# Optimization experiments

Hardware: AMD Instinct MI355X
Metric: run time of the kernel (lower is better)

## Reference

```python
import jax, jax.numpy as jnp
import numpy as np

B, IN_C, H, W = 32, 256, 32, 32
C_OUT, NUM_MODES, NEG_MODES, EMB = 256, 1, 3, 512
SIGMA, BETA, NEG_SCOPE, EPS = 0.5, 0.3, 2.0, 1e-12


def _l2norm(v, axis):
    return v / jnp.maximum(jnp.linalg.norm(v, axis=axis, keepdims=True), EPS)


def setup_inputs() -> dict:
    key = jax.random.key(0)
    ks = jax.random.split(key, 6)
    x = jax.random.normal(ks[0], (B, IN_C, H, W), jnp.float32)
    W_emb = jax.random.normal(ks[1], (EMB, IN_C), jnp.float32) * 0.02  # 1x1 conv kernel
    # rep_fc / neg_rep_fc: nn.Linear(1, C*modes*E), normal_init std=0.01
    rep_w = jax.random.normal(ks[2], (C_OUT * NUM_MODES * EMB, 1), jnp.float32) * 0.01
    rep_b = jax.random.normal(ks[3], (C_OUT * NUM_MODES * EMB,), jnp.float32) * 0.01
    neg_rep_w = jax.random.normal(ks[4], (C_OUT * NEG_MODES * EMB, 1), jnp.float32) * 0.01
    neg_rep_b = jax.random.normal(ks[5], (C_OUT * NEG_MODES * EMB,), jnp.float32) * 0.01
    return {"x": x, "W_emb": W_emb, "rep_w": rep_w, "rep_b": rep_b,
            "neg_rep_w": neg_rep_w, "neg_rep_b": neg_rep_b}


def reference(x, W_emb, rep_w, rep_b, neg_rep_w, neg_rep_b):
    # emb_module: 1x1 conv, then L2-normalize over channel dim (dim=1)
    emb = jnp.einsum('bchw,ec->behw', x, W_emb)
    emb = _l2norm(emb, axis=1)                                    # [B,E,H,W], unit-norm over E
    # training branch: reps = normalize(rep_fc(1.0)) = normalize(w*1 + b)
    reps = _l2norm((rep_w[:, 0] + rep_b).reshape(C_OUT, NUM_MODES, EMB), axis=2)
    reps_neg = _l2norm((neg_rep_w[:, 0] + neg_rep_b).reshape(C_OUT, NEG_MODES, EMB), axis=2)

    def dist(r):
        # ||e - r||^2 = ||e||^2 + ||r||^2 - 2 e.r = 2 - 2 e.r (both unit-norm)
        dot = jnp.einsum('behw,cme->bcmhw', emb, r)               # [B,C,M,H,W]
        return jnp.sqrt(jnp.maximum(2.0 - 2.0 * dot, 0.0))

    distances = dist(reps)                                        # [B,C,1,H,W]
    distances_neg = dist(reps_neg)                                # [B,C,3,H,W]
    inv2s2 = 1.0 / (2.0 * SIGMA ** 2)

    probs_neg = jnp.exp(-distances_neg ** 2 * inv2s2)
    cls_score_neg = probs_neg.max(axis=2)                         # [B,C,H,W]
    probs_ori = jnp.exp(-distances ** 2 * inv2s2).max(axis=2)     # [B,C,H,W]

    neg_min = distances_neg.min(axis=2, keepdims=True)            # [B,C,1,H,W]
    probs = jnp.exp(-(distances + BETA * jax.nn.relu(NEG_SCOPE - neg_min)) ** 2 * inv2s2)
    # cls_norm=True branch
    probs_sumj = probs.sum(axis=2)                                # [B,C,H,W]
    cls_score = probs_sumj / probs_sumj.sum(axis=1, keepdims=True)
    return (cls_score, cls_score_neg, distances, distances_neg, probs_ori)
```

## Files before the change

kernel.cpp:

```cpp
#include <hip/hip_runtime.h>
#include <stdint.h>

using s16x8 = __attribute__((ext_vector_type(8))) short;
using f32x4 = __attribute__((ext_vector_type(4))) float;

#define HW 1024
#define INC 256
#define EMB 512

#define OFF_CS 0
#define OFF_CN 8388608
#define OFF_D  16777216
#define OFF_DN 25165824
#define OFF_PO 50331648

__device__ __forceinline__ uint32_t f2bf(float f) {
  uint32_t u = __float_as_uint(f);
  return (u + 0x7FFFu + ((u >> 16) & 1u)) >> 16;
}
__device__ __forceinline__ int lswz(int row, int byte) {
  return byte ^ (((row >> 2) & 7) << 4);
}
__device__ __forceinline__ void gload16(const void* g, void* l) {
  __builtin_amdgcn_global_load_lds((const __attribute__((address_space(1))) uint32_t*)g,
                                   (__attribute__((address_space(3))) uint32_t*)l, 16, 0, 0);
}

__global__ __launch_bounds__(64) void k_prep(
    const float* __restrict__ rep_w, const float* __restrict__ rep_b,
    const float* __restrict__ neg_w, const float* __restrict__ neg_b,
    uint16_t* __restrict__ R, float* __restrict__ norms, float* __restrict__ psum) {
  int rb = blockIdx.x, lane = threadIdx.x;
  if (lane < 32) { norms[rb * 32 + lane] = 0.f; psum[rb * 32 + lane] = 0.f; }
  int c = rb >> 2, md = rb & 3;
  const float* w  = (md == 0) ? rep_w : neg_w;
  const float* bb = (md == 0) ? rep_b : neg_b;
  int base = (md == 0) ? c * EMB : (c * 3 + md - 1) * EMB;
  float v[8]; float ss = 0.f;
#pragma unroll
  for (int j = 0; j < 8; ++j) {
    float t = w[base + lane * 8 + j] + bb[base + lane * 8 + j];
    v[j] = t; ss += t * t;
  }
#pragma unroll
  for (int o = 1; o < 64; o <<= 1) ss += __shfl_xor(ss, o, 64);
  float inv = 1.f / fmaxf(sqrtf(ss), 1e-12f);
  uint16_t* dst = R + rb * EMB + lane * 8;
#pragma unroll
  for (int j = 0; j < 8; ++j) dst[j] = (uint16_t)f2bf(v[j] * inv);
}

__global__ __launch_bounds__(256) void k_gemm1(
    const float* __restrict__ x, const float* __restrict__ wemb,
    uint16_t* __restrict__ emb, float* __restrict__ norms) {
  int bid = blockIdx.x;
  int w = (bid & 7) * 128 + (bid >> 3);
  int e_tile = w & 3, px_tile = w >> 2;
  int e0 = e_tile * 128, px0 = px_tile * 128;
  int bimg = px0 >> 10, hw0 = px0 & 1023;
  int tid = threadIdx.x, lane = tid & 63, wid = tid >> 6;
  int wm = wid >> 1, wn = wid & 1, lr = lane & 15, lk = lane >> 4;
  __shared__ __align__(16) char smA[16384];
  __shared__ __align__(16) char smB[16384];
  f32x4 acc[4][4] = {};
  const float4* x4 = (const float4*)x;
  const float4* w4 = (const float4*)wemb;
  for (int kt = 0; kt < INC; kt += 64) {
    if (kt) __syncthreads();
#pragma unroll
    for (int i = 0; i < 4; ++i) {
      int p = tid + i * 256;
      int c2 = p >> 5, px4 = p & 31;
      int gi = ((bimg * INC + kt + c2 * 2) * HW + hw0) >> 2;
      float4 fa = x4[gi + px4];
      float4 fb = x4[gi + 256 + px4];
      float fa_[4] = {fa.x, fa.y, fa.z, fa.w};
      float fb_[4] = {fb.x, fb.y, fb.z, fb.w};
#pragma unroll
      for (int j = 0; j < 4; ++j) {
        int px = px4 * 4 + j;
        uint32_t val = f2bf(fa_[j]) | (f2bf(fb_[j]) << 16);
        *(uint32_t*)(smA + px * 128 + lswz(px, c2 * 4)) = val;
      }
    }
#pragma unroll
    for (int i = 0; i < 8; ++i) {
      int q = tid + i * 256;
      int er = q >> 4, c4 = q & 15;
      float4 f = w4[(((e0 + er) * INC + kt) >> 2) + c4];
      uint2 val;
      val.x = f2bf(f.x) | (f2bf(f.y) << 16);
      val.y = f2bf(f.z) | (f2bf(f.w) << 16);
      *(uint2*)(smB + er * 128 + lswz(er, c4 * 8)) = val;
    }
    __syncthreads();
#pragma unroll
    for (int kk = 0; kk < 64; kk += 32) {
      s16x8 a[4], b[4];
#pragma unroll
      for (int mi = 0; mi < 4; ++mi) {
        int row = wm * 64 + mi * 16 + lr;
        a[mi] = *(const s16x8*)(smA + row * 128 + lswz(row, (kk + lk * 8) * 2));
      }
#pragma unroll
      for (int ni = 0; ni < 4; ++ni) {
        int row = wn * 64 + ni * 16 + lr;
        b[ni] = *(const s16x8*)(smB + row * 128 + lswz(row, (kk + lk * 8) * 2));
      }
#pragma unroll
      for (int mi = 0; mi < 4; ++mi)
#pragma unroll
        for (int ni = 0; ni < 4; ++ni)
          acc[mi][ni] = __builtin_amdgcn_mfma_f32_16x16x32_bf16(a[mi], b[ni], acc[mi][ni], 0, 0, 0);
    }
  }
#pragma unroll
  for (int mi = 0; mi < 4; ++mi) {
#pragma unroll
    for (int r = 0; r < 4; ++r) {
      int pxg = px0 + wm * 64 + mi * 16 + lk * 4 + r;
      float ss = 0.f;
#pragma unroll
      for (int ni = 0; ni < 4; ++ni) {
        float v = acc[mi][ni][r];
        ss += v * v;
        uint32_t bf = f2bf(v);
        uint32_t other = (uint32_t)__shfl_xor((int)bf, 1, 64);
        if (!(lane & 1)) {
          int e = e0 + wn * 64 + ni * 16 + lr;
          *(uint32_t*)(emb + pxg * EMB + e) = bf | (other << 16);
        }
      }
#pragma unroll
      for (int o = 1; o < 16; o <<= 1) ss += __shfl_xor(ss, o, 64);
      if (lr == 0) atomicAdd(&norms[pxg], ss);
    }
  }
}

__global__ __launch_bounds__(256) void k_gemm2(
    const uint16_t* __restrict__ Rm, const uint16_t* __restrict__ emb,
    const float* __restrict__ norms, float* __restrict__ out, float* __restrict__ psum) {
  int bid = blockIdx.x;
  int w = (bid & 7) * 256 + (bid >> 3);
  int px_tile = w >> 3, rep_tile = w & 7;
  int px0 = px_tile * 128, r0 = rep_tile * 128;
  int bimg = px0 >> 10;
  int tid = threadIdx.x, lane = tid & 63, wid = tid >> 6;
  int wm = wid >> 1, wn = wid & 1, lr = lane & 15, lk = lane >> 4;
  __shared__ __align__(16) char smA[16384];
  __shared__ __align__(16) char smB[16384];
  f32x4 acc[4][4] = {};
  const char* Rb = (const char*)Rm;
  const char* Eb = (const char*)emb;
  int rowq = lane >> 3;
  int byteq = (lane & 7) * 16;
  for (int kt = 0; kt < EMB; kt += 64) {
    if (kt) __syncthreads();
#pragma unroll
    for (int i = 0; i < 4; ++i) {
      int chunk = wid + i * 4;
      int row = chunk * 8 + rowq;
      int sb = byteq ^ (((row >> 2) & 7) << 4);
      gload16(Rb + (r0 + row) * 1024 + kt * 2 + sb, smA + chunk * 1024);
      gload16(Eb + (px0 + row) * 1024 + kt * 2 + sb, smB + chunk * 1024);
    }
    __syncthreads();
#pragma unroll
    for (int kk = 0; kk < 64; kk += 32) {
      s16x8 a[4], b[4];
#pragma unroll
      for (int mi = 0; mi < 4; ++mi) {
        int row = wm * 64 + mi * 16 + lr;
        a[mi] = *(const s16x8*)(smA + row * 128 + lswz(row, (kk + lk * 8) * 2));
      }
#pragma unroll
      for (int ni = 0; ni < 4; ++ni) {
        int row = wn * 64 + ni * 16 + lr;
        b[ni] = *(const s16x8*)(smB + row * 128 + lswz(row, (kk + lk * 8) * 2));
      }
#pragma unroll
      for (int mi = 0; mi < 4; ++mi)
#pragma unroll
        for (int ni = 0; ni < 4; ++ni)
          acc[mi][ni] = __builtin_amdgcn_mfma_f32_16x16x32_bf16(a[mi], b[ni], acc[mi][ni], 0, 0, 0);
    }
  }
  float invn[4], psacc[4];
#pragma unroll
  for (int ni = 0; ni < 4; ++ni) {
    int px = px0 + wn * 64 + ni * 16 + lr;
    invn[ni] = rsqrtf(fmaxf(norms[px], 1e-24f));
    psacc[ni] = 0.f;
  }
#pragma unroll
  for (int mi = 0; mi < 4; ++mi) {
    int repb = r0 + wm * 64 + mi * 16 + lk * 4;
    int cls = repb >> 2;
#pragma unroll
    for (int ni = 0; ni < 4; ++ni) {
      int px = px0 + wn * 64 + ni * 16 + lr;
      int hw = px & 1023;
      float in = invn[ni];
      float d0 = acc[mi][ni][0] * in;
      float d1 = acc[mi][ni][1] * in;
      float d2 = acc[mi][ni][2] * in;
      float d3 = acc[mi][ni][3] * in;
      float q0 = fmaxf(2.f - 2.f * d0, 0.f);
      float q1 = fmaxf(2.f - 2.f * d1, 0.f);
      float q2 = fmaxf(2.f - 2.f * d2, 0.f);
      float q3 = fmaxf(2.f - 2.f * d3, 0.f);
      float dist0 = sqrtf(q0);
      float qmin = fminf(q1, fminf(q2, q3));
      float negmin = sqrtf(qmin);
      float p_ori = __expf(-2.f * q0);
      float cneg  = __expf(-2.f * qmin);
      float pen = 0.3f * fmaxf(2.f - negmin, 0.f);
      float tt = dist0 + pen;
      float probs = __expf(-2.f * tt * tt);
      int bo = (bimg * 256 + cls) * HW + hw;
      out[OFF_D + bo]  = dist0;
      out[OFF_PO + bo] = p_ori;
      out[OFF_CN + bo] = cneg;
      out[OFF_CS + bo] = probs;
      int bn = (bimg * 768 + cls * 3) * HW + hw;
      out[OFF_DN + bn]          = sqrtf(q1);
      out[OFF_DN + bn + HW]     = sqrtf(q2);
      out[OFF_DN + bn + 2 * HW] = sqrtf(q3);
      psacc[ni] += probs;
    }
  }
#pragma unroll
  for (int ni = 0; ni < 4; ++ni) {
    float s = psacc[ni];
    s += __shfl_xor(s, 16, 64);
    s += __shfl_xor(s, 32, 64);
    if (lk == 0) atomicAdd(&psum[px0 + wn * 64 + ni * 16 + lr], s);
  }
}

__global__ __launch_bounds__(256) void k_norm(float* __restrict__ out,
                                              const float* __restrict__ psum) {
  int idx4 = blockIdx.x * 256 + threadIdx.x;
  int base = idx4 << 2;
  int b = base >> 18, hw = base & 1023;
  float4 p = *(const float4*)&psum[(b << 10) | hw];
  float4* o4 = (float4*)out;
  float4 v = o4[idx4];
  v.x /= p.x; v.y /= p.y; v.z /= p.z; v.w /= p.w;
  o4[idx4] = v;
}

extern "C" void kernel_launch(void* const* d_in, const int* in_sizes, int n_in,
                              void* d_out, int out_size, void* d_ws, size_t ws_size,
                              hipStream_t stream) {
  (void)in_sizes; (void)n_in; (void)out_size; (void)ws_size;
  const float* x     = (const float*)d_in[0];
  const float* wemb  = (const float*)d_in[1];
  const float* rep_w = (const float*)d_in[2];
  const float* rep_b = (const float*)d_in[3];
  const float* neg_w = (const float*)d_in[4];
  const float* neg_b = (const float*)d_in[5];
  float* out = (float*)d_out;
  char* ws = (char*)d_ws;
  uint16_t* R     = (uint16_t*)ws;
  float*    norms = (float*)(ws + (1 << 20));
  float*    psum  = (float*)(ws + (1 << 20) + (1 << 17));
  uint16_t* emb   = (uint16_t*)(ws + (1 << 20) + (2 << 17));
  hipLaunchKernelGGL(k_prep,  dim3(1024), dim3(64),  0, stream,
                     rep_w, rep_b, neg_w, neg_b, R, norms, psum);
  hipLaunchKernelGGL(k_gemm1, dim3(1024), dim3(256), 0, stream, x, wemb, emb, norms);
  hipLaunchKernelGGL(k_gemm2, dim3(2048), dim3(256), 0, stream, R, emb, norms, out, psum);
  hipLaunchKernelGGL(k_norm,  dim3(8192), dim3(256), 0, stream, out, psum);
}
```

Measured before the change: 376.9 us.

## Stage gemm2 epilogue through LDS for float4 stores, replace atomics with partial buffers

The gemm2 epilogue now writes each of the seven output planes into a per-wave LDS scratch area and reads it back so every lane issues a coalesced float4 global store, instead of scattered scalar stores. The atomicAdd reductions for embedding norms and probability sums are replaced by plain writes into per-tile partial buffers, which consumers sum on read (8 partials in gemm2, 16 in k_norm). This also removes the zero-init in k_prep. The cost is extra LDS round-trips and a barrier in the epilogue, plus more partial-buffer reads and workspace.

```diff
diff --git a/kernel.cpp b/kernel.cpp
--- a/kernel.cpp
+++ b/kernel.cpp
@@ -7,6 +7,7 @@
 #define HW 1024
 #define INC 256
 #define EMB 512
+#define NPX 32768
 
 #define OFF_CS 0
 #define OFF_CN 8388608
@@ -29,9 +30,8 @@
 __global__ __launch_bounds__(64) void k_prep(
     const float* __restrict__ rep_w, const float* __restrict__ rep_b,
     const float* __restrict__ neg_w, const float* __restrict__ neg_b,
-    uint16_t* __restrict__ R, float* __restrict__ norms, float* __restrict__ psum) {
+    uint16_t* __restrict__ R) {
   int rb = blockIdx.x, lane = threadIdx.x;
-  if (lane < 32) { norms[rb * 32 + lane] = 0.f; psum[rb * 32 + lane] = 0.f; }
   int c = rb >> 2, md = rb & 3;
   const float* w  = (md == 0) ? rep_w : neg_w;
   const float* bb = (md == 0) ? rep_b : neg_b;
@@ -52,7 +52,7 @@
 
 __global__ __launch_bounds__(256) void k_gemm1(
     const float* __restrict__ x, const float* __restrict__ wemb,
-    uint16_t* __restrict__ emb, float* __restrict__ norms) {
+    uint16_t* __restrict__ emb, float* __restrict__ nparts) {
   int bid = blockIdx.x;
   int w = (bid & 7) * 128 + (bid >> 3);
   int e_tile = w & 3, px_tile = w >> 2;
@@ -131,16 +131,19 @@
           *(uint32_t*)(emb + pxg * EMB + e) = bf | (other << 16);
         }
       }
-#pragma unroll
-      for (int o = 1; o < 16; o <<= 1) ss += __shfl_xor(ss, o, 64);
-      if (lr == 0) atomicAdd(&norms[pxg], ss);
+      ss += __shfl_xor(ss, 1, 64);
+      ss += __shfl_xor(ss, 2, 64);
+      ss += __shfl_xor(ss, 4, 64);
+      ss += __shfl_xor(ss, 8, 64);
+      if (lr == 0) nparts[(e_tile * 2 + wn) * NPX + pxg] = ss;
     }
   }
 }
 
 __global__ __launch_bounds__(256) void k_gemm2(
     const uint16_t* __restrict__ Rm, const uint16_t* __restrict__ emb,
-    const float* __restrict__ norms, float* __restrict__ out, float* __restrict__ psum) {
+    const float* __restrict__ nparts, float* __restrict__ out,
+    float* __restrict__ psum_part) {
   int bid = blockIdx.x;
   int w = (bid & 7) * 256 + (bid >> 3);
   int px_tile = w >> 3, rep_tile = w & 7;
@@ -186,21 +189,27 @@
           acc[mi][ni] = __builtin_amdgcn_mfma_f32_16x16x32_bf16(a[mi], b[ni], acc[mi][ni], 0, 0, 0);
     }
   }
+  __syncthreads();
+  char* ep = smA + wid * 1184;
+  int hwbase = (px0 & 1023) + wn * 64;
+  int obase = (bimg * 256) * HW + hwbase;
   float invn[4], psacc[4];
 #pragma unroll
   for (int ni = 0; ni < 4; ++ni) {
     int px = px0 + wn * 64 + ni * 16 + lr;
-    invn[ni] = rsqrtf(fmaxf(norms[px], 1e-24f));
+    float s = 0.f;
+#pragma unroll
+    for (int t = 0; t < 8; ++t) s += nparts[t * NPX + px];
+    invn[ni] = rsqrtf(fmaxf(s, 1e-24f));
     psacc[ni] = 0.f;
   }
 #pragma unroll
   for (int mi = 0; mi < 4; ++mi) {
-    int repb = r0 + wm * 64 + mi * 16 + lk * 4;
-    int cls = repb >> 2;
+    int clsl = wm * 16 + mi * 4 + lk;
+    int cls = (r0 >> 2) + clsl;
+    float pl[7][4];
 #pragma unroll
     for (int ni = 0; ni < 4; ++ni) {
-      int px = px0 + wn * 64 + ni * 16 + lr;
-      int hw = px & 1023;
       float in = invn[ni];
       float d0 = acc[mi][ni][0] * in;
       float d1 = acc[mi][ni][1] * in;
@@ -213,21 +222,29 @@
       float dist0 = sqrtf(q0);
       float qmin = fminf(q1, fminf(q2, q3));
       float negmin = sqrtf(qmin);
-      float p_ori = __expf(-2.f * q0);
-      float cneg  = __expf(-2.f * qmin);
       float pen = 0.3f * fmaxf(2.f - negmin, 0.f);
       float tt = dist0 + pen;
       float probs = __expf(-2.f * tt * tt);
-      int bo = (bimg * 256 + cls) * HW + hw;
-      out[OFF_D + bo]  = dist0;
-      out[OFF_PO + bo] = p_ori;
-      out[OFF_CN + bo] = cneg;
-      out[OFF_CS + bo] = probs;
-      int bn = (bimg * 768 + cls * 3) * HW + hw;
-      out[OFF_DN + bn]          = sqrtf(q1);
-      out[OFF_DN + bn + HW]     = sqrtf(q2);
-      out[OFF_DN + bn + 2 * HW] = sqrtf(q3);
+      pl[0][ni] = probs;
+      pl[1][ni] = __expf(-2.f * qmin);
+      pl[2][ni] = dist0;
+      pl[3][ni] = sqrtf(q1);
+      pl[4][ni] = sqrtf(q2);
+      pl[5][ni] = sqrtf(q3);
+      pl[6][ni] = __expf(-2.f * q0);
       psacc[ni] += probs;
+    }
+    int bc = obase + cls * HW;
+    int bn = OFF_DN + (bimg * 768 + cls * 3) * HW + hwbase;
+    int pbase[7] = { OFF_CS + bc, OFF_CN + bc, OFF_D + bc,
+                     bn, bn + HW, bn + 2 * HW, OFF_PO + bc };
+#pragma unroll
+    for (int p = 0; p < 7; ++p) {
+#pragma unroll
+      for (int ni = 0; ni < 4; ++ni)
+        *(float*)(ep + lk * 288 + (ni * 16 + lr) * 4) = pl[p][ni];
+      float4 v = *(const float4*)(ep + lk * 288 + lr * 16);
+      *(float4*)(&out[pbase[p] + 4 * lr]) = v;
     }
   }
 #pragma unroll
@@ -235,19 +252,26 @@
     float s = psacc[ni];
     s += __shfl_xor(s, 16, 64);
     s += __shfl_xor(s, 32, 64);
-    if (lk == 0) atomicAdd(&psum[px0 + wn * 64 + ni * 16 + lr], s);
+    if (lk == 0)
+      psum_part[(rep_tile * 2 + wm) * NPX + px0 + wn * 64 + ni * 16 + lr] = s;
   }
 }
 
 __global__ __launch_bounds__(256) void k_norm(float* __restrict__ out,
-                                              const float* __restrict__ psum) {
+                                              const float* __restrict__ psum_part) {
   int idx4 = blockIdx.x * 256 + threadIdx.x;
   int base = idx4 << 2;
   int b = base >> 18, hw = base & 1023;
-  float4 p = *(const float4*)&psum[(b << 10) | hw];
+  int pxb = (b << 10) | hw;
+  float sx = 0.f, sy = 0.f, sz = 0.f, sw = 0.f;
+#pragma unroll
+  for (int t = 0; t < 16; ++t) {
+    float4 p = *(const float4*)&psum_part[t * NPX + pxb];
+    sx += p.x; sy += p.y; sz += p.z; sw += p.w;
+  }
   float4* o4 = (float4*)out;
   float4 v = o4[idx4];
-  v.x /= p.x; v.y /= p.y; v.z /= p.z; v.w /= p.w;
+  v.x /= sx; v.y /= sy; v.z /= sz; v.w /= sw;
   o4[idx4] = v;
 }
 
@@ -263,13 +287,13 @@
   const float* neg_b = (const float*)d_in[5];
   float* out = (float*)d_out;
   char* ws = (char*)d_ws;
-  uint16_t* R     = (uint16_t*)ws;
-  float*    norms = (float*)(ws + (1 << 20));
-  float*    psum  = (float*)(ws + (1 << 20) + (1 << 17));
-  uint16_t* emb   = (uint16_t*)(ws + (1 << 20) + (2 << 17));
+  uint16_t* R         = (uint16_t*)ws;
+  float*    nparts    = (float*)(ws + (1 << 20));
+  float*    psum_part = (float*)(ws + (2 << 20));
+  uint16_t* emb       = (uint16_t*)(ws + (4 << 20));
   hipLaunchKernelGGL(k_prep,  dim3(1024), dim3(64),  0, stream,
-                     rep_w, rep_b, neg_w, neg_b, R, norms, psum);
-  hipLaunchKernelGGL(k_gemm1, dim3(1024), dim3(256), 0, stream, x, wemb, emb, norms);
-  hipLaunchKernelGGL(k_gemm2, dim3(2048), dim3(256), 0, stream, R, emb, norms, out, psum);
-  hipLaunchKernelGGL(k_norm,  dim3(8192), dim3(256), 0, stream, out, psum);
-}
+                     rep_w, rep_b, neg_w, neg_b, R);
+  hipLaunchKernelGGL(k_gemm1, dim3(1024), dim3(256), 0, stream, x, wemb, emb, nparts);
+  hipLaunchKernelGGL(k_gemm2, dim3(2048), dim3(256), 0, stream, R, emb, nparts, out, psum_part);
+  hipLaunchKernelGGL(k_norm,  dim3(8192), dim3(256), 0, stream, out, psum_part);
+}
```

Result: no change. 376.4 us (-0.1%).
